# Kernel tuning notes

Hardware: AMD Instinct MI355X
Metric: run time of the kernel (lower is better)

The kernel has to match this reference:

```python
import jax, jax.numpy as jnp
import numpy as np

NUM_HEAD = 16
FEAT_DIM = 1024
HEAD_DIM = FEAT_DIM // NUM_HEAD  # 64
MAX_SEQ_LEN = 2048
BATCH = 2


def setup_inputs() -> dict:
    key = jax.random.key(0)
    ks = jax.random.split(key, 6)
    x = jax.random.normal(ks[0], (BATCH, MAX_SEQ_LEN, FEAT_DIM), dtype=jnp.float32)
    # xavier_uniform: limit = sqrt(6/(fan_in+fan_out)); torch Linear weight is [out, in]
    def xavier(k, out_f, in_f):
        lim = float(np.sqrt(6.0 / (in_f + out_f)))
        return jax.random.uniform(k, (out_f, in_f), dtype=jnp.float32, minval=-lim, maxval=lim)
    W1 = xavier(ks[1], HEAD_DIM, HEAD_DIM)          # attn_mlp[0].weight
    b1 = jnp.zeros((HEAD_DIM,), dtype=jnp.float32)
    W2 = xavier(ks[2], MAX_SEQ_LEN, HEAD_DIM)       # attn_mlp[2].weight
    b2 = jnp.zeros((MAX_SEQ_LEN,), dtype=jnp.float32)
    Wv = xavier(ks[3], FEAT_DIM, FEAT_DIM)          # value_linear.weight (no bias)
    Wo = xavier(ks[4], FEAT_DIM, FEAT_DIM)          # output_linear.weight (no bias)
    return {"x": x, "W1": W1, "b1": b1, "W2": W2, "b2": b2, "Wv": Wv, "Wo": Wo}


def _split_head(t):
    b, n, _ = t.shape
    return t.reshape(b, n, NUM_HEAD, HEAD_DIM).transpose(0, 2, 1, 3)  # [b,h,n,d]


def reference(x, W1, b1, W2, b2, Wv, Wo):
    # value projection (dropout is identity in eval / p=0)
    value = x @ Wv.T                                   # [b,n,F]
    vh = _split_head(value)                            # [b,h,n,d]
    xh = _split_head(x)                                # [b,h,n,d]
    # per-head MLP -> dense attention logits [b,h,n,max_seq_len]
    hid = jax.nn.relu(jnp.einsum('bhnd,ed->bhne', xh, W1) + b1)
    logits = jnp.einsum('bhne,me->bhnm', hid, W2) + b2
    attn = jax.nn.softmax(logits, axis=-1)             # [b,h,n,m]
    out_h = jnp.einsum('bhnm,bhmd->bhnd', attn, vh)    # m == seq_len
    b_, h_, n_, d_ = out_h.shape
    out = out_h.transpose(0, 2, 1, 3).reshape(b_, n_, FEAT_DIM)
    return out @ Wo.T
```

## Files before the change

### kernel.cpp

```cpp
#include <hip/hip_runtime.h>
#include <hip/hip_bf16.h>
#include <math.h>
#include <stdint.h>


typedef __attribute__((ext_vector_type(8))) short bf16x8;
typedef __attribute__((ext_vector_type(4))) float f32x4;
typedef __attribute__((ext_vector_type(16))) float f32x16;

#define LOG2E 1.4426950408889634f

__device__ __forceinline__ unsigned short f2bf(float f) {
  union { float f; unsigned u; } v; v.f = f;
  unsigned r = v.u + 0x7FFFu + ((v.u >> 16) & 1u);
  return (unsigned short)(r >> 16);
}

__global__ __launch_bounds__(256) void conv_bf16(const float* __restrict__ src,
                                                 unsigned short* __restrict__ dst, int nq) {
  int stride = gridDim.x * blockDim.x;
  for (int q = blockIdx.x * blockDim.x + threadIdx.x; q < nq; q += stride) {
    float4 v = *(const float4*)(src + (size_t)q * 4);
    unsigned short p0 = f2bf(v.x), p1 = f2bf(v.y), p2 = f2bf(v.z), p3 = f2bf(v.w);
    uint2 u;
    u.x = (unsigned)p0 | ((unsigned)p1 << 16);
    u.y = (unsigned)p2 | ((unsigned)p3 << 16);
    *(uint2*)(dst + (size_t)q * 4) = u;
  }
}

__global__ __launch_bounds__(256) void b2l_kernel(const float* __restrict__ src,
                                                  float* __restrict__ dst, int n) {
  int i = blockIdx.x * blockDim.x + threadIdx.x;
  if (i < n) dst[i] = src[i] * LOG2E;
}

__device__ __forceinline__ void stage64(const char* g, size_t ldbytes, char* lds,
                                        int w, int lane) {
#pragma unroll
  for (int t = 0; t < 2; ++t) {
    int row  = w * 16 + t * 8 + (lane >> 3);
    int csrc = (lane & 7) ^ (lane >> 3);
    const char* src = g + (size_t)row * ldbytes + (csrc << 4);
    char* dst = lds + ((w * 2 + t) << 10);
    __builtin_amdgcn_global_load_lds((const __attribute__((address_space(1))) void*)src,
                                     (__attribute__((address_space(3))) void*)dst,
                                     16, 0, 0);
  }
}

__device__ __forceinline__ bf16x8 rdfrag(const char* lds, int row, int kt, int lane) {
  int c = ((kt << 2) + (lane >> 4)) ^ (row & 7);
  return *(const bf16x8*)(lds + row * 128 + (c << 4));
}

__device__ __forceinline__ bf16x8 rdfrag32(const char* lds, int row, int chunk) {
  int c = chunk ^ (row & 7);
  return *(const bf16x8*)(lds + row * 128 + (c << 4));
}

__device__ __forceinline__ f32x16 loadb16(const float* p) {
  f32x16 r;
#pragma unroll
  for (int qd = 0; qd < 4; ++qd) {
    float4 v = *(const float4*)(p + qd * 8);
    r[qd * 4 + 0] = v.x; r[qd * 4 + 1] = v.y; r[qd * 4 + 2] = v.z; r[qd * 4 + 3] = v.w;
  }
  return r;
}

__device__ __forceinline__ bf16x8 pk_swap(float r0, float r1, float r2, float r3,
                                          float r4, float r5, float r6, float r7) {
  unsigned a, b, c, d;
  asm("v_cvt_pk_bf16_f32 %0, %1, %2" : "=v"(a) : "v"(r0), "v"(r1));
  asm("v_cvt_pk_bf16_f32 %0, %1, %2" : "=v"(b) : "v"(r4), "v"(r5));
  asm("v_cvt_pk_bf16_f32 %0, %1, %2" : "=v"(c) : "v"(r2), "v"(r3));
  asm("v_cvt_pk_bf16_f32 %0, %1, %2" : "=v"(d) : "v"(r6), "v"(r7));
  asm("v_permlane32_swap_b32 %0, %1" : "+v"(a), "+v"(b));
  asm("v_permlane32_swap_b32 %0, %1" : "+v"(c), "+v"(d));
  union { unsigned u[4]; bf16x8 v; } r;
  r.u[0] = a; r.u[1] = c; r.u[2] = b; r.u[3] = d;
  return r.v;
}

template<int MODE>
__global__ __launch_bounds__(256) void gemm_bt(const unsigned short* __restrict__ A,
                                               const unsigned short* __restrict__ B,
                                               void* __restrict__ C, int K) {
  __shared__ __attribute__((aligned(16))) char As[8192];
  __shared__ __attribute__((aligned(16))) char Bs[8192];
  int tid = threadIdx.x, w = tid >> 6, lane = tid & 63;
  int bm = blockIdx.x, bn = blockIdx.y;
  const char* Ab = (const char*)A + (size_t)bm * 64 * (K * 2);
  const char* Bb = (const char*)B + (size_t)bn * 64 * (K * 2);
  f32x4 acc[4] = {};
  int nsteps = K >> 6;
  for (int kk = 0; kk < nsteps; ++kk) {
    __syncthreads();
    stage64(Ab + (size_t)kk * 128, (size_t)K * 2, As, w, lane);
    stage64(Bb + (size_t)kk * 128, (size_t)K * 2, Bs, w, lane);
    __syncthreads();
#pragma unroll
    for (int kt = 0; kt < 2; ++kt) {
      bf16x8 a = rdfrag(As, w * 16 + (lane & 15), kt, lane);
#pragma unroll
      for (int nj = 0; nj < 4; ++nj) {
        bf16x8 b = rdfrag(Bs, nj * 16 + (lane & 15), kt, lane);
        acc[nj] = __builtin_amdgcn_mfma_f32_16x16x32_bf16(a, b, acc[nj], 0, 0, 0);
      }
    }
  }
  int g = lane >> 4, fr = lane & 15;
  if (MODE == 0) {
    unsigned short* vt = (unsigned short*)C;
    int growbase = bm * 64 + w * 16 + g * 4;
    int b = growbase >> 11;
    int n = growbase & 2047;
#pragma unroll
    for (int nj = 0; nj < 4; ++nj) {
      int d = nj * 16 + fr;
      unsigned short p0 = f2bf(acc[nj][0]), p1 = f2bf(acc[nj][1]);
      unsigned short p2 = f2bf(acc[nj][2]), p3 = f2bf(acc[nj][3]);
      uint2 u;
      u.x = (unsigned)p0 | ((unsigned)p1 << 16);
      u.y = (unsigned)p2 | ((unsigned)p3 << 16);
      *(uint2*)(vt + ((size_t)((b * 16 + bn) * 64 + d)) * 2048 + n) = u;
    }
  } else {
    float* Cf = (float*)C;
    int grow = bm * 64 + w * 16 + g * 4;
#pragma unroll
    for (int nj = 0; nj < 4; ++nj) {
#pragma unroll
      for (int r = 0; r < 4; ++r) {
        Cf[(size_t)(grow + r) * 1024 + bn * 64 + nj * 16 + fr] = acc[nj][r];
      }
    }
  }
}

__global__ __launch_bounds__(256) void flash_kernel(const unsigned short* __restrict__ xb,
                                                    const unsigned short* __restrict__ w1b,
                                                    const float* __restrict__ b1,
                                                    const unsigned short* __restrict__ w2b,
                                                    const float* __restrict__ b2l,
                                                    const unsigned short* __restrict__ vt,
                                                    unsigned short* __restrict__ aout) {
  __shared__ __attribute__((aligned(16))) char Kbuf[16384];
  __shared__ __attribute__((aligned(16))) char Vbuf[16384];
  int tid = threadIdx.x, w = tid >> 6, lane = tid & 63;
  int l31 = lane & 31, hi = lane >> 5;
  int f = blockIdx.x;
  int swz = ((f & 7) << 6) | (f >> 3);
  int qt = swz & 15, bh = swz >> 4;
  int b = bh >> 4, h = bh & 15;

  const char* px = (const char*)(xb + ((size_t)(b * 2048 + qt * 128)) * 1024 + h * 64);
  stage64(px, 2048, Kbuf, w, lane);
  stage64(px + (size_t)64 * 2048, 2048, Kbuf + 8192, w, lane);
  stage64((const char*)w1b, 128, Vbuf, w, lane);
  __syncthreads();

  f32x16 h0 = loadb16(b1 + hi * 4);
  f32x16 h1 = loadb16(b1 + 32 + hi * 4);
#pragma unroll
  for (int ks = 0; ks < 4; ++ks) {
    bf16x8 xf = rdfrag32(Kbuf, w * 32 + l31, ks * 2 + hi);
    bf16x8 wf0 = rdfrag32(Vbuf, l31, ks * 2 + hi);
    h0 = __builtin_amdgcn_mfma_f32_32x32x16_bf16(wf0, xf, h0, 0, 0, 0);
    bf16x8 wf1 = rdfrag32(Vbuf, 32 + l31, ks * 2 + hi);
    h1 = __builtin_amdgcn_mfma_f32_32x32x16_bf16(wf1, xf, h1, 0, 0, 0);
  }
#pragma unroll
  for (int i = 0; i < 16; ++i) {
    h0[i] = fmaxf(h0[i], 0.f) * LOG2E;
    h1[i] = fmaxf(h1[i], 0.f) * LOG2E;
  }
  bf16x8 qb[4];
  qb[0] = pk_swap(h0[0], h0[1], h0[2], h0[3], h0[4], h0[5], h0[6], h0[7]);
  qb[1] = pk_swap(h0[8], h0[9], h0[10], h0[11], h0[12], h0[13], h0[14], h0[15]);
  qb[2] = pk_swap(h1[0], h1[1], h1[2], h1[3], h1[4], h1[5], h1[6], h1[7]);
  qb[3] = pk_swap(h1[8], h1[9], h1[10], h1[11], h1[12], h1[13], h1[14], h1[15]);
  __syncthreads();

  const char* vtb = (const char*)vt + (size_t)bh * 64 * 4096;
  stage64((const char*)w2b, 128, Kbuf, w, lane);
  stage64(vtb, 4096, Vbuf, w, lane);
  float4 pre[8];
#pragma unroll
  for (int pq = 0; pq < 4; ++pq) {
    pre[pq]     = *(const float4*)(b2l + pq * 8 + hi * 4);
    pre[pq + 4] = *(const float4*)(b2l + 32 + pq * 8 + hi * 4);
  }
  f32x16 oA = {}, oB = {};
  float lrs0 = 0.f, lrs1 = 0.f, lrs2 = 0.f, lrs3 = 0.f;
  __syncthreads();

  for (int mt = 0; mt < 32; ++mt) {
    int cur = mt & 1;
    const char* Kc = Kbuf + (cur << 13);
    const char* Vc = Vbuf + (cur << 13);
    if (mt < 31) {
      stage64((const char*)w2b + (size_t)(mt + 1) * 8192, 128, Kbuf + ((cur ^ 1) << 13), w, lane);
      stage64(vtb + (size_t)(mt + 1) * 128, 4096, Vbuf + ((cur ^ 1) << 13), w, lane);
    }
    f32x16 s0, s1;
#pragma unroll
    for (int qd = 0; qd < 4; ++qd) {
      s0[qd * 4 + 0] = pre[qd].x;     s0[qd * 4 + 1] = pre[qd].y;
      s0[qd * 4 + 2] = pre[qd].z;     s0[qd * 4 + 3] = pre[qd].w;
      s1[qd * 4 + 0] = pre[qd + 4].x; s1[qd * 4 + 1] = pre[qd + 4].y;
      s1[qd * 4 + 2] = pre[qd + 4].z; s1[qd * 4 + 3] = pre[qd + 4].w;
    }
#pragma unroll
    for (int kt = 0; kt < 4; ++kt) {
      bf16x8 kf0 = rdfrag32(Kc, l31, kt * 2 + hi);
      s0 = __builtin_amdgcn_mfma_f32_32x32x16_bf16(kf0, qb[kt], s0, 0, 0, 0);
      bf16x8 kf1 = rdfrag32(Kc, 32 + l31, kt * 2 + hi);
      s1 = __builtin_amdgcn_mfma_f32_32x32x16_bf16(kf1, qb[kt], s1, 0, 0, 0);
    }
    if (mt < 31) {
#pragma unroll
      for (int pq = 0; pq < 4; ++pq) {
        pre[pq]     = *(const float4*)(b2l + (mt + 1) * 64 + pq * 8 + hi * 4);
        pre[pq + 4] = *(const float4*)(b2l + (mt + 1) * 64 + 32 + pq * 8 + hi * 4);
      }
    }
#pragma unroll
    for (int i = 0; i < 16; ++i) {
      float t0, t1;
      asm("v_exp_f32 %0, %1" : "=v"(t0) : "v"(s0[i]));
      asm("v_exp_f32 %0, %1" : "=v"(t1) : "v"(s1[i]));
      s0[i] = t0; s1[i] = t1;
      if ((i & 3) == 0) { lrs0 += t0; lrs0 += t1; }
      else if ((i & 3) == 1) { lrs1 += t0; lrs1 += t1; }
      else if ((i & 3) == 2) { lrs2 += t0; lrs2 += t1; }
      else { lrs3 += t0; lrs3 += t1; }
    }
    bf16x8 pa[4];
    pa[0] = pk_swap(s0[0], s0[1], s0[2], s0[3], s0[4], s0[5], s0[6], s0[7]);
    pa[1] = pk_swap(s0[8], s0[9], s0[10], s0[11], s0[12], s0[13], s0[14], s0[15]);
    pa[2] = pk_swap(s1[0], s1[1], s1[2], s1[3], s1[4], s1[5], s1[6], s1[7]);
    pa[3] = pk_swap(s1[8], s1[9], s1[10], s1[11], s1[12], s1[13], s1[14], s1[15]);
#pragma unroll
    for (int ks = 0; ks < 4; ++ks) {
      bf16x8 vf0 = rdfrag32(Vc, l31, ks * 2 + hi);
      oA = __builtin_amdgcn_mfma_f32_32x32x16_bf16(pa[ks], vf0, oA, 0, 0, 0);
      bf16x8 vf1 = rdfrag32(Vc, 32 + l31, ks * 2 + hi);
      oB = __builtin_amdgcn_mfma_f32_32x32x16_bf16(pa[ks], vf1, oB, 0, 0, 0);
    }
    __syncthreads();
  }

  float l = (lrs0 + lrs1) + (lrs2 + lrs3);
  l += __shfl_xor(l, 32);
  float inv = 1.f / l;
  float iv[16];
#pragma unroll
  for (int r = 0; r < 16; ++r)
    iv[r] = __shfl(inv, (r & 3) + 8 * (r >> 2) + 4 * hi);
  int nb = qt * 128 + w * 32;
#pragma unroll
  for (int r = 0; r < 16; ++r) {
    int ql = (r & 3) + 8 * (r >> 2) + 4 * hi;
    size_t off = ((size_t)(b * 2048 + nb + ql)) * 1024 + h * 64 + l31;
    aout[off]      = f2bf(oA[r] * iv[r]);
    aout[off + 32] = f2bf(oB[r] * iv[r]);
  }
}

extern "C" void kernel_launch(void* const* d_in, const int* in_sizes, int n_in,
                              void* d_out, int out_size, void* d_ws, size_t ws_size,
                              hipStream_t stream) {
  (void)in_sizes; (void)n_in; (void)out_size; (void)ws_size;
  const float* x  = (const float*)d_in[0];
  const float* W1 = (const float*)d_in[1];
  const float* b1 = (const float*)d_in[2];
  const float* W2 = (const float*)d_in[3];
  const float* b2 = (const float*)d_in[4];
  const float* Wv = (const float*)d_in[5];
  const float* Wo = (const float*)d_in[6];
  float* out = (float*)d_out;

  char* ws = (char*)d_ws;
  unsigned short* xb   = (unsigned short*)(ws);
  unsigned short* wvb  = (unsigned short*)(ws +  8388608);
  unsigned short* wob  = (unsigned short*)(ws + 10485760);
  unsigned short* w2b  = (unsigned short*)(ws + 12582912);
  unsigned short* w1b  = (unsigned short*)(ws + 12845056);
  float*          b2l  = (float*)         (ws + 12853248);
  unsigned short* vt   = (unsigned short*)(ws + 21233664);
  unsigned short* aout = (unsigned short*)(ws + 29622272);

  conv_bf16<<<1024, 256, 0, stream>>>(x,  xb,  4194304 / 4);
  conv_bf16<<<1024, 256, 0, stream>>>(Wv, wvb, 1048576 / 4);
  conv_bf16<<<1024, 256, 0, stream>>>(Wo, wob, 1048576 / 4);
  conv_bf16<<< 128, 256, 0, stream>>>(W2, w2b,  131072 / 4);
  conv_bf16<<<   4, 256, 0, stream>>>(W1, w1b,    4096 / 4);
  b2l_kernel<<<   8, 256, 0, stream>>>(b2, b2l, 2048);

  gemm_bt<0><<<dim3(64, 16), 256, 0, stream>>>(xb, wvb, (void*)vt, 1024);
  flash_kernel<<<512, 256, 0, stream>>>(xb, w1b, b1, w2b, b2l, vt, aout);
  gemm_bt<1><<<dim3(64, 16), 256, 0, stream>>>(aout, wob, (void*)out, 1024);
}
```

Baseline: 110.7 us.

## Use 128x128 double-buffered GEMMs, fold exp(b2) into V, merge prep kernels

New measurement: 101.5 us. -8.3%, faster.

```diff
diff --git a/kernel.cpp b/kernel.cpp
--- a/kernel.cpp
+++ b/kernel.cpp
@@ -21,18 +21,49 @@
   int stride = gridDim.x * blockDim.x;
   for (int q = blockIdx.x * blockDim.x + threadIdx.x; q < nq; q += stride) {
     float4 v = *(const float4*)(src + (size_t)q * 4);
-    unsigned short p0 = f2bf(v.x), p1 = f2bf(v.y), p2 = f2bf(v.z), p3 = f2bf(v.w);
     uint2 u;
-    u.x = (unsigned)p0 | ((unsigned)p1 << 16);
-    u.y = (unsigned)p2 | ((unsigned)p3 << 16);
+    u.x = (unsigned)f2bf(v.x) | ((unsigned)f2bf(v.y) << 16);
+    u.y = (unsigned)f2bf(v.z) | ((unsigned)f2bf(v.w) << 16);
     *(uint2*)(dst + (size_t)q * 4) = u;
   }
 }
 
-__global__ __launch_bounds__(256) void b2l_kernel(const float* __restrict__ src,
-                                                  float* __restrict__ dst, int n) {
-  int i = blockIdx.x * blockDim.x + threadIdx.x;
-  if (i < n) dst[i] = src[i] * LOG2E;
+__global__ __launch_bounds__(256) void prep_kernel(const float* __restrict__ Wv,
+                                                   const float* __restrict__ Wo,
+                                                   const float* __restrict__ W2,
+                                                   const float* __restrict__ W1,
+                                                   const float* __restrict__ b2,
+                                                   unsigned short* __restrict__ wvb,
+                                                   unsigned short* __restrict__ wob,
+                                                   unsigned short* __restrict__ w2b,
+                                                   unsigned short* __restrict__ w1b,
+                                                   float* __restrict__ eb2f,
+                                                   unsigned short* __restrict__ ebb) {
+  int bid = blockIdx.x;
+  if (bid == 1024) {
+    int i = threadIdx.x;
+#pragma unroll
+    for (int t = 0; t < 8; ++t) {
+      int k = i * 8 + t;
+      float e = __expf(b2[k]);
+      eb2f[k] = e;
+      ebb[k] = f2bf(e);
+    }
+    return;
+  }
+  int stride = 1024 * 256;
+  for (int q = bid * 256 + threadIdx.x; q < 558080; q += stride) {
+    const float* s; unsigned short* d; int o;
+    if (q < 262144)      { s = Wv; d = wvb; o = q; }
+    else if (q < 524288) { s = Wo; d = wob; o = q - 262144; }
+    else if (q < 557056) { s = W2; d = w2b; o = q - 524288; }
+    else                 { s = W1; d = w1b; o = q - 557056; }
+    float4 v = *(const float4*)(s + (size_t)o * 4);
+    uint2 u;
+    u.x = (unsigned)f2bf(v.x) | ((unsigned)f2bf(v.y) << 16);
+    u.y = (unsigned)f2bf(v.z) | ((unsigned)f2bf(v.w) << 16);
+    *(uint2*)(d + (size_t)o * 4) = u;
+  }
 }
 
 __device__ __forceinline__ void stage64(const char* g, size_t ldbytes, char* lds,
@@ -47,11 +78,6 @@
                                      (__attribute__((address_space(3))) void*)dst,
                                      16, 0, 0);
   }
-}
-
-__device__ __forceinline__ bf16x8 rdfrag(const char* lds, int row, int kt, int lane) {
-  int c = ((kt << 2) + (lane >> 4)) ^ (row & 7);
-  return *(const bf16x8*)(lds + row * 128 + (c << 4));
 }
 
 __device__ __forceinline__ bf16x8 rdfrag32(const char* lds, int row, int chunk) {
@@ -84,57 +110,86 @@
 }
 
 template<int MODE>
-__global__ __launch_bounds__(256) void gemm_bt(const unsigned short* __restrict__ A,
+__global__ __launch_bounds__(256) void gemm128(const unsigned short* __restrict__ A,
                                                const unsigned short* __restrict__ B,
-                                               void* __restrict__ C, int K) {
-  __shared__ __attribute__((aligned(16))) char As[8192];
-  __shared__ __attribute__((aligned(16))) char Bs[8192];
+                                               void* __restrict__ C,
+                                               const float* __restrict__ eb2f, int K) {
+  __shared__ __attribute__((aligned(16))) char As[2][16384];
+  __shared__ __attribute__((aligned(16))) char Bs[2][16384];
   int tid = threadIdx.x, w = tid >> 6, lane = tid & 63;
+  int l31 = lane & 31, hi = lane >> 5;
+  int wr = w >> 1, wc = w & 1;
   int bm = blockIdx.x, bn = blockIdx.y;
-  const char* Ab = (const char*)A + (size_t)bm * 64 * (K * 2);
-  const char* Bb = (const char*)B + (size_t)bn * 64 * (K * 2);
-  f32x4 acc[4] = {};
-  int nsteps = K >> 6;
-  for (int kk = 0; kk < nsteps; ++kk) {
+  const char* Ab = (const char*)A + (size_t)bm * 128 * (K * 2);
+  const char* Bb = (const char*)B + (size_t)bn * 128 * (K * 2);
+  size_t ld = (size_t)K * 2;
+
+  f32x16 acc00 = {}, acc01 = {}, acc10 = {}, acc11 = {};
+  stage64(Ab, ld, As[0], w, lane);
+  stage64(Ab + 64 * ld, ld, As[0] + 8192, w, lane);
+  stage64(Bb, ld, Bs[0], w, lane);
+  stage64(Bb + 64 * ld, ld, Bs[0] + 8192, w, lane);
+  __syncthreads();
+
+  int nst = K >> 6;
+  for (int kk = 0; kk < nst; ++kk) {
+    int cur = kk & 1;
+    if (kk + 1 < nst) {
+      const char* An = Ab + (size_t)(kk + 1) * 128;
+      const char* Bn = Bb + (size_t)(kk + 1) * 128;
+      stage64(An, ld, As[cur ^ 1], w, lane);
+      stage64(An + 64 * ld, ld, As[cur ^ 1] + 8192, w, lane);
+      stage64(Bn, ld, Bs[cur ^ 1], w, lane);
+      stage64(Bn + 64 * ld, ld, Bs[cur ^ 1] + 8192, w, lane);
+    }
+    __builtin_amdgcn_s_setprio(1);
+#pragma unroll
+    for (int ks = 0; ks < 4; ++ks) {
+      bf16x8 a0 = rdfrag32(As[cur], wr * 64 + l31, ks * 2 + hi);
+      bf16x8 a1 = rdfrag32(As[cur], wr * 64 + 32 + l31, ks * 2 + hi);
+      bf16x8 b0 = rdfrag32(Bs[cur], wc * 64 + l31, ks * 2 + hi);
+      bf16x8 b1 = rdfrag32(Bs[cur], wc * 64 + 32 + l31, ks * 2 + hi);
+      acc00 = __builtin_amdgcn_mfma_f32_32x32x16_bf16(a0, b0, acc00, 0, 0, 0);
+      acc01 = __builtin_amdgcn_mfma_f32_32x32x16_bf16(a0, b1, acc01, 0, 0, 0);
+      acc10 = __builtin_amdgcn_mfma_f32_32x32x16_bf16(a1, b0, acc10, 0, 0, 0);
+      acc11 = __builtin_amdgcn_mfma_f32_32x32x16_bf16(a1, b1, acc11, 0, 0, 0);
+    }
+    __builtin_amdgcn_s_setprio(0);
     __syncthreads();
-    stage64(Ab + (size_t)kk * 128, (size_t)K * 2, As, w, lane);
-    stage64(Bb + (size_t)kk * 128, (size_t)K * 2, Bs, w, lane);
-    __syncthreads();
-#pragma unroll
-    for (int kt = 0; kt < 2; ++kt) {
-      bf16x8 a = rdfrag(As, w * 16 + (lane & 15), kt, lane);
-#pragma unroll
-      for (int nj = 0; nj < 4; ++nj) {
-        bf16x8 b = rdfrag(Bs, nj * 16 + (lane & 15), kt, lane);
-        acc[nj] = __builtin_amdgcn_mfma_f32_16x16x32_bf16(a, b, acc[nj], 0, 0, 0);
-      }
-    }
-  }
-  int g = lane >> 4, fr = lane & 15;
+  }
+
   if (MODE == 0) {
     unsigned short* vt = (unsigned short*)C;
-    int growbase = bm * 64 + w * 16 + g * 4;
-    int b = growbase >> 11;
-    int n = growbase & 2047;
-#pragma unroll
-    for (int nj = 0; nj < 4; ++nj) {
-      int d = nj * 16 + fr;
-      unsigned short p0 = f2bf(acc[nj][0]), p1 = f2bf(acc[nj][1]);
-      unsigned short p2 = f2bf(acc[nj][2]), p3 = f2bf(acc[nj][3]);
-      uint2 u;
-      u.x = (unsigned)p0 | ((unsigned)p1 << 16);
-      u.y = (unsigned)p2 | ((unsigned)p3 << 16);
-      *(uint2*)(vt + ((size_t)((b * 16 + bn) * 64 + d)) * 2048 + n) = u;
+#pragma unroll
+    for (int i = 0; i < 2; ++i) {
+      int rowb = bm * 128 + wr * 64 + i * 32;
+#pragma unroll
+      for (int qd = 0; qd < 4; ++qd) {
+        int m0 = rowb + qd * 8 + hi * 4;
+        float4 e4 = *(const float4*)(eb2f + (m0 & 2047));
+        int bb = m0 >> 11, n = m0 & 2047;
+#pragma unroll
+        for (int j = 0; j < 2; ++j) {
+          int h = bn * 2 + wc, d = j * 32 + l31;
+          f32x16 a = (i == 0) ? (j == 0 ? acc00 : acc01) : (j == 0 ? acc10 : acc11);
+          int r0 = qd * 4;
+          uint2 u;
+          u.x = (unsigned)f2bf(a[r0] * e4.x) | ((unsigned)f2bf(a[r0 + 1] * e4.y) << 16);
+          u.y = (unsigned)f2bf(a[r0 + 2] * e4.z) | ((unsigned)f2bf(a[r0 + 3] * e4.w) << 16);
+          *(uint2*)(vt + ((size_t)((bb * 16 + h) * 64 + d)) * 2048 + n) = u;
+        }
+      }
     }
   } else {
     float* Cf = (float*)C;
-    int grow = bm * 64 + w * 16 + g * 4;
-#pragma unroll
-    for (int nj = 0; nj < 4; ++nj) {
-#pragma unroll
-      for (int r = 0; r < 4; ++r) {
-        Cf[(size_t)(grow + r) * 1024 + bn * 64 + nj * 16 + fr] = acc[nj][r];
-      }
+    int rb = bm * 128 + wr * 64, cb = bn * 128 + wc * 64;
+#pragma unroll
+    for (int r = 0; r < 16; ++r) {
+      int row = (r & 3) + 8 * (r >> 2) + 4 * hi;
+      Cf[(size_t)(rb + row) * 1024 + cb + l31]          = acc00[r];
+      Cf[(size_t)(rb + row) * 1024 + cb + 32 + l31]     = acc01[r];
+      Cf[(size_t)(rb + 32 + row) * 1024 + cb + l31]     = acc10[r];
+      Cf[(size_t)(rb + 32 + row) * 1024 + cb + 32 + l31] = acc11[r];
     }
   }
 }
@@ -143,7 +198,7 @@
                                                     const unsigned short* __restrict__ w1b,
                                                     const float* __restrict__ b1,
                                                     const unsigned short* __restrict__ w2b,
-                                                    const float* __restrict__ b2l,
+                                                    const unsigned short* __restrict__ ebb,
                                                     const unsigned short* __restrict__ vt,
                                                     unsigned short* __restrict__ aout) {
   __shared__ __attribute__((aligned(16))) char Kbuf[16384];
@@ -186,14 +241,9 @@
   const char* vtb = (const char*)vt + (size_t)bh * 64 * 4096;
   stage64((const char*)w2b, 128, Kbuf, w, lane);
   stage64(vtb, 4096, Vbuf, w, lane);
-  float4 pre[8];
-#pragma unroll
-  for (int pq = 0; pq < 4; ++pq) {
-    pre[pq]     = *(const float4*)(b2l + pq * 8 + hi * 4);
-    pre[pq + 4] = *(const float4*)(b2l + 32 + pq * 8 + hi * 4);
-  }
-  f32x16 oA = {}, oB = {};
-  float lrs0 = 0.f, lrs1 = 0.f, lrs2 = 0.f, lrs3 = 0.f;
+
+  const f32x16 zro = {};
+  f32x16 oA = {}, oB = {}, L = {};
   __syncthreads();
 
   for (int mt = 0; mt < 32; ++mt) {
@@ -204,14 +254,13 @@
       stage64((const char*)w2b + (size_t)(mt + 1) * 8192, 128, Kbuf + ((cur ^ 1) << 13), w, lane);
       stage64(vtb + (size_t)(mt + 1) * 128, 4096, Vbuf + ((cur ^ 1) << 13), w, lane);
     }
-    f32x16 s0, s1;
-#pragma unroll
-    for (int qd = 0; qd < 4; ++qd) {
-      s0[qd * 4 + 0] = pre[qd].x;     s0[qd * 4 + 1] = pre[qd].y;
-      s0[qd * 4 + 2] = pre[qd].z;     s0[qd * 4 + 3] = pre[qd].w;
-      s1[qd * 4 + 0] = pre[qd + 4].x; s1[qd * 4 + 1] = pre[qd + 4].y;
-      s1[qd * 4 + 2] = pre[qd + 4].z; s1[qd * 4 + 3] = pre[qd + 4].w;
-    }
+    bf16x8 ebf0 = *(const bf16x8*)(ebb + mt * 64 + hi * 8);
+    bf16x8 ebf1 = *(const bf16x8*)(ebb + mt * 64 + 16 + hi * 8);
+    bf16x8 ebf2 = *(const bf16x8*)(ebb + mt * 64 + 32 + hi * 8);
+    bf16x8 ebf3 = *(const bf16x8*)(ebb + mt * 64 + 48 + hi * 8);
+
+    f32x16 s0 = zro, s1 = zro;
+    __builtin_amdgcn_s_setprio(1);
 #pragma unroll
     for (int kt = 0; kt < 4; ++kt) {
       bf16x8 kf0 = rdfrag32(Kc, l31, kt * 2 + hi);
@@ -219,53 +268,54 @@
       bf16x8 kf1 = rdfrag32(Kc, 32 + l31, kt * 2 + hi);
       s1 = __builtin_amdgcn_mfma_f32_32x32x16_bf16(kf1, qb[kt], s1, 0, 0, 0);
     }
-    if (mt < 31) {
-#pragma unroll
-      for (int pq = 0; pq < 4; ++pq) {
-        pre[pq]     = *(const float4*)(b2l + (mt + 1) * 64 + pq * 8 + hi * 4);
-        pre[pq + 4] = *(const float4*)(b2l + (mt + 1) * 64 + 32 + pq * 8 + hi * 4);
-      }
-    }
+    __builtin_amdgcn_s_setprio(0);
 #pragma unroll
     for (int i = 0; i < 16; ++i) {
       float t0, t1;
       asm("v_exp_f32 %0, %1" : "=v"(t0) : "v"(s0[i]));
       asm("v_exp_f32 %0, %1" : "=v"(t1) : "v"(s1[i]));
       s0[i] = t0; s1[i] = t1;
-      if ((i & 3) == 0) { lrs0 += t0; lrs0 += t1; }
-      else if ((i & 3) == 1) { lrs1 += t0; lrs1 += t1; }
-      else if ((i & 3) == 2) { lrs2 += t0; lrs2 += t1; }
-      else { lrs3 += t0; lrs3 += t1; }
-    }
-    bf16x8 pa[4];
-    pa[0] = pk_swap(s0[0], s0[1], s0[2], s0[3], s0[4], s0[5], s0[6], s0[7]);
-    pa[1] = pk_swap(s0[8], s0[9], s0[10], s0[11], s0[12], s0[13], s0[14], s0[15]);
-    pa[2] = pk_swap(s1[0], s1[1], s1[2], s1[3], s1[4], s1[5], s1[6], s1[7]);
-    pa[3] = pk_swap(s1[8], s1[9], s1[10], s1[11], s1[12], s1[13], s1[14], s1[15]);
-#pragma unroll
-    for (int ks = 0; ks < 4; ++ks) {
-      bf16x8 vf0 = rdfrag32(Vc, l31, ks * 2 + hi);
-      oA = __builtin_amdgcn_mfma_f32_32x32x16_bf16(pa[ks], vf0, oA, 0, 0, 0);
-      bf16x8 vf1 = rdfrag32(Vc, 32 + l31, ks * 2 + hi);
-      oB = __builtin_amdgcn_mfma_f32_32x32x16_bf16(pa[ks], vf1, oB, 0, 0, 0);
-    }
+    }
+    bf16x8 pa0 = pk_swap(s0[0], s0[1], s0[2], s0[3], s0[4], s0[5], s0[6], s0[7]);
+    bf16x8 pa1 = pk_swap(s0[8], s0[9], s0[10], s0[11], s0[12], s0[13], s0[14], s0[15]);
+    bf16x8 pa2 = pk_swap(s1[0], s1[1], s1[2], s1[3], s1[4], s1[5], s1[6], s1[7]);
+    bf16x8 pa3 = pk_swap(s1[8], s1[9], s1[10], s1[11], s1[12], s1[13], s1[14], s1[15]);
+    __builtin_amdgcn_s_setprio(1);
+    L = __builtin_amdgcn_mfma_f32_32x32x16_bf16(pa0, ebf0, L, 0, 0, 0);
+    L = __builtin_amdgcn_mfma_f32_32x32x16_bf16(pa1, ebf1, L, 0, 0, 0);
+    L = __builtin_amdgcn_mfma_f32_32x32x16_bf16(pa2, ebf2, L, 0, 0, 0);
+    L = __builtin_amdgcn_mfma_f32_32x32x16_bf16(pa3, ebf3, L, 0, 0, 0);
+    {
+      bf16x8 vf;
+      vf = rdfrag32(Vc, l31, 0 + hi);
+      oA = __builtin_amdgcn_mfma_f32_32x32x16_bf16(pa0, vf, oA, 0, 0, 0);
+      vf = rdfrag32(Vc, 32 + l31, 0 + hi);
+      oB = __builtin_amdgcn_mfma_f32_32x32x16_bf16(pa0, vf, oB, 0, 0, 0);
+      vf = rdfrag32(Vc, l31, 2 + hi);
+      oA = __builtin_amdgcn_mfma_f32_32x32x16_bf16(pa1, vf, oA, 0, 0, 0);
+      vf = rdfrag32(Vc, 32 + l31, 2 + hi);
+      oB = __builtin_amdgcn_mfma_f32_32x32x16_bf16(pa1, vf, oB, 0, 0, 0);
+      vf = rdfrag32(Vc, l31, 4 + hi);
+      oA = __builtin_amdgcn_mfma_f32_32x32x16_bf16(pa2, vf, oA, 0, 0, 0);
+      vf = rdfrag32(Vc, 32 + l31, 4 + hi);
+      oB = __builtin_amdgcn_mfma_f32_32x32x16_bf16(pa2, vf, oB, 0, 0, 0);
+      vf = rdfrag32(Vc, l31, 6 + hi);
+      oA = __builtin_amdgcn_mfma_f32_32x32x16_bf16(pa3, vf, oA, 0, 0, 0);
+      vf = rdfrag32(Vc, 32 + l31, 6 + hi);
+      oB = __builtin_amdgcn_mfma_f32_32x32x16_bf16(pa3, vf, oB, 0, 0, 0);
+    }
+    __builtin_amdgcn_s_setprio(0);
     __syncthreads();
   }
 
-  float l = (lrs0 + lrs1) + (lrs2 + lrs3);
-  l += __shfl_xor(l, 32);
-  float inv = 1.f / l;
-  float iv[16];
-#pragma unroll
-  for (int r = 0; r < 16; ++r)
-    iv[r] = __shfl(inv, (r & 3) + 8 * (r >> 2) + 4 * hi);
   int nb = qt * 128 + w * 32;
 #pragma unroll
   for (int r = 0; r < 16; ++r) {
+    float iv = 1.f / L[r];
     int ql = (r & 3) + 8 * (r >> 2) + 4 * hi;
     size_t off = ((size_t)(b * 2048 + nb + ql)) * 1024 + h * 64 + l31;
-    aout[off]      = f2bf(oA[r] * iv[r]);
-    aout[off + 32] = f2bf(oB[r] * iv[r]);
+    aout[off]      = f2bf(oA[r] * iv);
+    aout[off + 32] = f2bf(oB[r] * iv);
   }
 }
 
@@ -288,18 +338,16 @@
   unsigned short* wob  = (unsigned short*)(ws + 10485760);
   unsigned short* w2b  = (unsigned short*)(ws + 12582912);
   unsigned short* w1b  = (unsigned short*)(ws + 12845056);
-  float*          b2l  = (float*)         (ws + 12853248);
+  float*          eb2f = (float*)         (ws + 12853248);
+  unsigned short* ebb  = (unsigned short*)(ws + 12861440);
   unsigned short* vt   = (unsigned short*)(ws + 21233664);
   unsigned short* aout = (unsigned short*)(ws + 29622272);
 
-  conv_bf16<<<1024, 256, 0, stream>>>(x,  xb,  4194304 / 4);
-  conv_bf16<<<1024, 256, 0, stream>>>(Wv, wvb, 1048576 / 4);
-  conv_bf16<<<1024, 256, 0, stream>>>(Wo, wob, 1048576 / 4);
-  conv_bf16<<< 128, 256, 0, stream>>>(W2, w2b,  131072 / 4);
-  conv_bf16<<<   4, 256, 0, stream>>>(W1, w1b,    4096 / 4);
-  b2l_kernel<<<   8, 256, 0, stream>>>(b2, b2l, 2048);
-
-  gemm_bt<0><<<dim3(64, 16), 256, 0, stream>>>(xb, wvb, (void*)vt, 1024);
-  flash_kernel<<<512, 256, 0, stream>>>(xb, w1b, b1, w2b, b2l, vt, aout);
-  gemm_bt<1><<<dim3(64, 16), 256, 0, stream>>>(aout, wob, (void*)out, 1024);
-}
+  conv_bf16<<<1024, 256, 0, stream>>>(x, xb, 4194304 / 4);
+  prep_kernel<<<1025, 256, 0, stream>>>(Wv, Wo, W2, W1, b2,
+                                        wvb, wob, w2b, w1b, eb2f, ebb);
+
+  gemm128<0><<<dim3(32, 8), 256, 0, stream>>>(xb, wvb, (void*)vt, eb2f, 1024);
+  flash_kernel<<<512, 256, 0, stream>>>(xb, w1b, b1, w2b, ebb, vt, aout);
+  gemm128<1><<<dim3(32, 8), 256, 0, stream>>>(aout, wob, (void*)out, eb2f, 1024);
+}
```
